# Optimization experiments

Hardware: AMD Instinct MI355X
Metric: run time of the kernel (lower is better)

The kernel has to match this reference:

```python
import jax, jax.numpy as jnp
import numpy as np

EPS = 1e-5
NUM_GROUPS = 16


def _deform_conv(x, offset, mask, weight):
    """Modulated deformable conv v2, 3x3, stride 1, pad 1, no bias.
    x: [B,C,H,W], offset: [B,18,H,W] (y,x interleaved per kernel point),
    mask: [B,9,H,W], weight: [O,C,3,3].
    """
    B, C, H, W = x.shape
    O = weight.shape[0]
    K = 9
    off = offset.reshape(B, K, 2, H, W)
    dy, dx = off[:, :, 0], off[:, :, 1]  # [B,K,H,W]
    # base sampling grid: output pixel + kernel tap offset (pad=1 -> taps -1..1)
    ky, kx = jnp.meshgrid(jnp.arange(3), jnp.arange(3), indexing='ij')
    ky = (ky.reshape(K) - 1).astype(x.dtype)
    kx = (kx.reshape(K) - 1).astype(x.dtype)
    iy = jnp.arange(H, dtype=x.dtype)[:, None]
    ix = jnp.arange(W, dtype=x.dtype)[None, :]
    py = iy[None, None] + ky[None, :, None, None] + dy  # [B,K,H,W]
    px = ix[None, None] + kx[None, :, None, None] + dx

    y0 = jnp.floor(py)
    x0 = jnp.floor(px)
    wy = py - y0  # grad flows to offsets via these weights
    wx = px - x0

    xf = x.reshape(B, C, H * W)

    def gather(yc, xc, w):
        # yc,xc,w: [B,K,H,W] float; returns weighted samples [B,C,K,H,W]
        valid = (yc >= 0) & (yc <= H - 1) & (xc >= 0) & (xc <= W - 1)
        yi = jnp.clip(yc, 0, H - 1).astype(jnp.int32)
        xi = jnp.clip(xc, 0, W - 1).astype(jnp.int32)
        idx = (yi * W + xi).reshape(B, K * H * W)
        g = jax.vmap(lambda xb, ib: xb[:, ib])(xf, idx)  # [B,C,K*H*W]
        g = g.reshape(B, C, K, H, W)
        wv = (w * valid.astype(x.dtype))[:, None]  # [B,1,K,H,W]
        return g * wv

    val = gather(y0, x0, (1 - wy) * (1 - wx))
    val = val + gather(y0, x0 + 1, (1 - wy) * wx)
    val = val + gather(y0 + 1, x0, wy * (1 - wx))
    val = val + gather(y0 + 1, x0 + 1, wy * wx)

    val = val * mask[:, None]  # modulation: [B,C,K,H,W] * [B,1,K,H,W]
    w = weight.reshape(O, C, K)
    return jnp.einsum('bckhw,ock->bohw', val, w)


def _group_norm(y, gamma, beta):
    B, O, H, W = y.shape
    g = y.reshape(B, NUM_GROUPS, O // NUM_GROUPS, H, W)
    mean = g.mean(axis=(2, 3, 4), keepdims=True)
    var = ((g - mean) ** 2).mean(axis=(2, 3, 4), keepdims=True)
    g = (g - mean) * jax.lax.rsqrt(var + EPS)
    y = g.reshape(B, O, H, W)
    return y * gamma[None, :, None, None] + beta[None, :, None, None]


def setup_inputs() -> dict:
    key = jax.random.key(0)
    k1, k2, k3, k4 = jax.random.split(key, 4)
    B, C, O, H, W = 8, 256, 256, 64, 64
    x = jax.random.normal(k1, (B, C, H, W), jnp.float32)
    offset = jax.random.normal(k2, (B, 18, H, W), jnp.float32)
    mask = jax.random.uniform(k3, (B, 9, H, W), jnp.float32)
    weight = jax.random.normal(k4, (O, C, 3, 3), jnp.float32) * 0.02
    gamma = jnp.ones((O,), jnp.float32)
    beta = jnp.zeros((O,), jnp.float32)
    return {"x": x, "offset": offset, "mask": mask, "weight": weight,
            "gamma": gamma, "beta": beta}


def reference(x, offset, mask, weight, gamma, beta):
    y = _deform_conv(x, offset, mask, weight)
    return _group_norm(y, gamma, beta)
```

## Files before the change

### kernel.cpp

```cpp
#include <hip/hip_runtime.h>
#include <hip/hip_fp16.h>
#include <math.h>

#define BB 8
#define CC 256
#define OO 256
#define HH 64
#define WW 64
#define KK 9
#define HWSZ 4096
#define CKSZ 2304
#define NG 16
#define OPG 16
#define EPSV 1e-5f

typedef _Float16 f16;
typedef f16 f16x8 __attribute__((ext_vector_type(8)));
typedef float f32x4 __attribute__((ext_vector_type(4)));

#define XH_ELEMS ((size_t)BB*HWSZ*CC)
#define WF_ELEMS ((size_t)OO*CKSZ)
#define CV_ELEMS ((size_t)BB*OO*HWSZ)
#define NSTRIP 32

__global__ __launch_bounds__(256) void x_transpose_k(
    const float* __restrict__ x, __half* __restrict__ xh)
{
  int blk = blockIdx.x;
  int b = blk >> 8; int rem = blk & 255;
  int c0 = (rem >> 6) * 64; int hw0 = (rem & 63) * 64;
  __shared__ float st[64][65];
  int t = threadIdx.x;
  #pragma unroll
  for (int i = 0; i < 16; ++i) {
    int idx = t + i*256; int c = idx >> 6, w = idx & 63;
    st[c][w] = x[((size_t)(b*CC + c0 + c))*HWSZ + hw0 + w];
  }
  __syncthreads();
  #pragma unroll
  for (int i = 0; i < 8; ++i) {
    int idx = t + i*256; int r = idx >> 5, cp = idx & 31;
    __half2 v = __floats2half2_rn(st[cp*2][r], st[cp*2+1][r]);
    *(__half2*)&xh[((size_t)(b*HWSZ) + hw0 + r)*CC + c0 + cp*2] = v;
  }
}

__global__ __launch_bounds__(256) void w_frag_k(
    const float* __restrict__ w, __half* __restrict__ wf)
{
  int i = blockIdx.x*256 + threadIdx.x;
  int e = i & 7, lane = (i >> 3) & 63, mi = (i >> 9) & 3;
  int ks = (i >> 11) & 1, wm = (i >> 12) & 3, cc = i >> 14;
  int k = cc >> 2, c0i = cc & 3;
  int o = wm*64 + mi*16 + (lane & 15);
  int c = c0i*64 + ks*32 + (lane >> 4)*8 + e;
  wf[i] = __float2half(w[(o*CC + c)*KK + k]);
}

template<int F16OUT>
__global__ __launch_bounds__(512, 2) void dcn_mfma_k(
    const float* __restrict__ off, const float* __restrict__ msk,
    const __half* __restrict__ xh, const __half* __restrict__ wf,
    float* __restrict__ out32, __half* __restrict__ conv16,
    float* __restrict__ psum)
{
  __shared__ __half sVl[2][128*64];
  __shared__ uint   sTapP[KK][128][4];

  const int t = threadIdx.x;
  const int b = blockIdx.x & 7;
  const int strip = blockIdx.x >> 3;
  const int h0 = strip * 2;

  const int lane = t & 63, wid = t >> 6;
  const int lr = lane & 15, lh = lane >> 4;
  const int gp = t >> 2, gq = t & 3;

  auto load_A = [&](int cc, f16x8 a[2][2]) {
    #pragma unroll
    for (int ks = 0; ks < 2; ++ks)
      #pragma unroll
      for (int mi = 0; mi < 2; ++mi) {
        int omi = wid*2 + mi;
        const __half* ap = wf + (size_t)(cc*4 + (omi >> 2))*4096
                              + (size_t)(ks*4 + (omi & 3))*512 + lane*8;
        a[ks][mi] = *(const f16x8*)ap;
      }
  };

  f16x8 aregA[2][2], aregB[2][2];
  load_A(0, aregA);

  for (int s = t; s < KK*128; s += 512) {
    int k = s >> 7, p = s & 127;
    int h = h0 + (p >> 6), w = p & 63;
    float dy = off[(((b*18) + 2*k    )*HH + h)*WW + w];
    float dx = off[(((b*18) + 2*k + 1)*HH + h)*WW + w];
    float m  = msk[(((b*KK) + k)*HH + h)*WW + w];
    float py = (float)(h + (k/3) - 1) + dy;
    float px = (float)(w + (k%3) - 1) + dx;
    float y0f = floorf(py), x0f = floorf(px);
    float wy = py - y0f, wx = px - x0f;
    int y0 = (int)y0f, x0 = (int)x0f;
    #pragma unroll
    for (int tap = 0; tap < 4; ++tap) {
      int yy = y0 + (tap >> 1), xx = x0 + (tap & 1);
      bool v = (yy >= 0) & (yy < HH) & (xx >= 0) & (xx < WW);
      float bw = ((tap >> 1) ? wy : 1.f - wy) * ((tap & 1) ? wx : 1.f - wx);
      float wgt = v ? bw * m : 0.f;
      int cy = min(max(yy, 0), HH-1), cx = min(max(xx, 0), WW-1);
      uint idx = (uint)(cy*WW + cx);
      sTapP[k][p][tap] = (idx << 16)
                       | (uint)__half_as_ushort(__float2half(wgt));
    }
  }
  __syncthreads();

  f32x4 acc[2][8];
  #pragma unroll
  for (int mi = 0; mi < 2; ++mi)
    #pragma unroll
    for (int ni = 0; ni < 8; ++ni) acc[mi][ni] = (f32x4){0.f,0.f,0.f,0.f};

  const char* xbase = (const char*)xh + (size_t)b * (HWSZ*CC*2);

  uint toff[4]; __half2 twv[4];
  #pragma unroll
  for (int i = 0; i < 4; ++i) {
    uint tp = sTapP[0][gp][i];
    toff[i] = (tp >> 16) << 9;
    twv[i]  = __half2half2(__ushort_as_half((unsigned short)(tp & 0xFFFFu)));
  }
  int tk = 0;

  auto combine_write = [&](uint4 r0, uint4 r1, uint4 r2, uint4 r3,
                           int oct, __half* dst) {
    const __half2* t0 = (const __half2*)&r0; const __half2* t1 = (const __half2*)&r1;
    const __half2* t2 = (const __half2*)&r2; const __half2* t3 = (const __half2*)&r3;
    __half2 o_[4];
    #pragma unroll
    for (int r = 0; r < 4; ++r)
      o_[r] = __hfma2(twv[0], t0[r], __hfma2(twv[1], t1[r],
              __hfma2(twv[2], t2[r], __hmul2(twv[3], t3[r]))));
    *(uint4*)&dst[gp*64 + ((oct ^ (gp & 7)) << 3)] = *(uint4*)o_;
  };

  {
    const char* cb = xbase + gq*16;
    uint4 a0 = *(const uint4*)(cb + toff[0]);
    uint4 a1 = *(const uint4*)(cb + toff[1]);
    uint4 a2 = *(const uint4*)(cb + toff[2]);
    uint4 a3 = *(const uint4*)(cb + toff[3]);
    uint4 b0 = *(const uint4*)(cb + toff[0] + 64);
    uint4 b1 = *(const uint4*)(cb + toff[1] + 64);
    uint4 b2 = *(const uint4*)(cb + toff[2] + 64);
    uint4 b3 = *(const uint4*)(cb + toff[3] + 64);
    combine_write(a0, a1, a2, a3, gq,     sVl[0]);
    combine_write(b0, b1, b2, b3, gq + 4, sVl[0]);
  }

  int cur = 0;

  auto do_chunk = [&](int cc, f16x8 aCur[2][2], f16x8 aNxt[2][2]) {
    __syncthreads();

    bool pf = (cc + 1 < 36);
    int kn = (cc+1) >> 2, c0n = ((cc+1) & 3) << 6;
    uint4 ga0, ga1, ga2, ga3, gb0, gb1, gb2, gb3;
    if (pf) {
      load_A(cc + 1, aNxt);
      if (kn != tk) {
        #pragma unroll
        for (int i = 0; i < 4; ++i) {
          uint tp = sTapP[kn][gp][i];
          toff[i] = (tp >> 16) << 9;
          twv[i]  = __half2half2(__ushort_as_half((unsigned short)(tp & 0xFFFFu)));
        }
        tk = kn;
      }
      const char* cb = xbase + (size_t)(c0n*2) + gq*16;
      ga0 = *(const uint4*)(cb + toff[0]);
      ga1 = *(const uint4*)(cb + toff[1]);
      ga2 = *(const uint4*)(cb + toff[2]);
      ga3 = *(const uint4*)(cb + toff[3]);
      gb0 = *(const uint4*)(cb + toff[0] + 64);
      gb1 = *(const uint4*)(cb + toff[1] + 64);
      gb2 = *(const uint4*)(cb + toff[2] + 64);
      gb3 = *(const uint4*)(cb + toff[3] + 64);
    }

    #pragma unroll
    for (int ks = 0; ks < 2; ++ks) {
      f16x8 brg[8];
      #pragma unroll
      for (int ni = 0; ni < 8; ++ni) {
        int r = ni*16 + lr;
        brg[ni] = *(const f16x8*)&sVl[cur][r*64 + (((ks*4 + lh) ^ (r & 7)) << 3)];
      }
      #pragma unroll
      for (int mi = 0; mi < 2; ++mi)
        #pragma unroll
        for (int ni = 0; ni < 8; ++ni)
          acc[mi][ni] = __builtin_amdgcn_mfma_f32_16x16x32_f16(
              aCur[ks][mi], brg[ni], acc[mi][ni], 0, 0, 0);
    }

    if (pf) {
      combine_write(ga0, ga1, ga2, ga3, gq,     sVl[cur ^ 1]);
      combine_write(gb0, gb1, gb2, gb3, gq + 4, sVl[cur ^ 1]);
      cur ^= 1;
    }
  };

  #pragma unroll 1
  for (int cc2 = 0; cc2 < 36; cc2 += 2) {
    do_chunk(cc2,     aregA, aregB);
    do_chunk(cc2 + 1, aregB, aregA);
  }

  #pragma unroll
  for (int mi = 0; mi < 2; ++mi) {
    #pragma unroll
    for (int ni = 0; ni < 8; ++ni) {
      int ob = wid*32 + mi*16 + lh*4;
      int pp = ni*16 + lr;
      #pragma unroll
      for (int j = 0; j < 4; ++j) {
        size_t idx = ((size_t)(b*OO + ob + j))*HWSZ + strip*128 + pp;
        if (F16OUT) conv16[idx] = __float2half(acc[mi][ni][j]);
        else        out32[idx] = acc[mi][ni][j];
      }
    }
  }

  if (F16OUT) {
    #pragma unroll
    for (int mi = 0; mi < 2; ++mi) {
      float s1 = 0.f, s2 = 0.f;
      #pragma unroll
      for (int ni = 0; ni < 8; ++ni)
        #pragma unroll
        for (int j = 0; j < 4; ++j) {
          float v = acc[mi][ni][j];
          s1 += v; s2 += v*v;
        }
      #pragma unroll
      for (int d = 32; d > 0; d >>= 1) {
        s1 += __shfl_xor(s1, d);
        s2 += __shfl_xor(s2, d);
      }
      if (lane == 0) {
        int g = wid*2 + mi;
        psum[(size_t)blockIdx.x*32 + g*2]     = s1;
        psum[(size_t)blockIdx.x*32 + g*2 + 1] = s2;
      }
    }
  }
}

__global__ __launch_bounds__(256) void gn_norm2_k(
    const __half* __restrict__ conv16, const float* __restrict__ psum,
    const float* __restrict__ gamma, const float* __restrict__ beta,
    float* __restrict__ out)
{
  int bid = blockIdx.x;
  int bo = bid >> 1;
  int b = bo >> 8, o = bo & 255;
  int g = o >> 4;
  float s1 = 0.f, s2 = 0.f;
  for (int st = 0; st < NSTRIP; ++st) {
    s1 += psum[(size_t)(st*8 + b)*32 + g*2];
    s2 += psum[(size_t)(st*8 + b)*32 + g*2 + 1];
  }
  const float invN = 1.f / (float)(OPG*HWSZ);
  float mean = s1 * invN;
  float var  = s2 * invN - mean*mean;
  float inv = rsqrtf(var + EPSV);
  float sc = gamma[o]*inv;
  float sh = beta[o] - mean*sc;

  size_t e0 = ((size_t)(b*OO + o))*HWSZ + (size_t)(bid & 1)*2048
            + (size_t)threadIdx.x*8;
  uint4 u = *(const uint4*)(conv16 + e0);
  const __half2* hh = (const __half2*)&u;
  float r[8];
  #pragma unroll
  for (int j = 0; j < 4; ++j) {
    float2 f = __half22float2(hh[j]);
    r[2*j] = f.x; r[2*j+1] = f.y;
  }
  *(float4*)&out[e0]     = make_float4(r[0]*sc+sh, r[1]*sc+sh, r[2]*sc+sh, r[3]*sc+sh);
  *(float4*)&out[e0 + 4] = make_float4(r[4]*sc+sh, r[5]*sc+sh, r[6]*sc+sh, r[7]*sc+sh);
}

__global__ __launch_bounds__(1024) void gn_stats_k(
    const float* __restrict__ out, float* __restrict__ stats)
{
  int bg = blockIdx.x;
  const float4* p = (const float4*)(out + (size_t)bg*OPG*HWSZ);
  const int n4 = OPG*HWSZ/4;
  float s1 = 0.f, s2 = 0.f;
  for (int i = threadIdx.x; i < n4; i += 1024) {
    float4 v = p[i];
    s1 += v.x + v.y + v.z + v.w;
    s2 += v.x*v.x + v.y*v.y + v.z*v.z + v.w*v.w;
  }
  #pragma unroll
  for (int o2 = 32; o2 > 0; o2 >>= 1) {
    s1 += __shfl_down(s1, o2);
    s2 += __shfl_down(s2, o2);
  }
  __shared__ float r1[16], r2[16];
  int wd = threadIdx.x >> 6, lane = threadIdx.x & 63;
  if (lane == 0) { r1[wd] = s1; r2[wd] = s2; }
  __syncthreads();
  if (threadIdx.x == 0) {
    float t1 = 0.f, t2 = 0.f;
    #pragma unroll
    for (int i = 0; i < 16; i++) { t1 += r1[i]; t2 += r2[i]; }
    const float invN = 1.f / (float)(OPG*HWSZ);
    float mean = t1 * invN;
    float var  = t2 * invN - mean*mean;
    stats[bg*2]   = mean;
    stats[bg*2+1] = var;
  }
}

__global__ __launch_bounds__(256) void gn_norm_k(
    float* __restrict__ out, const float* __restrict__ stats,
    const float* __restrict__ gamma, const float* __restrict__ beta)
{
  size_t i = (size_t)blockIdx.x*256 + threadIdx.x;
  const size_t n4 = (size_t)BB*OO*HWSZ/4;
  if (i >= n4) return;
  size_t base = i*4;
  int bo = (int)(base / HWSZ);
  int b = bo / OO, o = bo - b*OO;
  int g = o >> 4;
  float mean = stats[(b*NG+g)*2], var = stats[(b*NG+g)*2+1];
  float inv = rsqrtf(var + EPSV);
  float sc = gamma[o]*inv;
  float sh = beta[o] - mean*sc;
  float4 v = *(float4*)&out[base];
  v.x = v.x*sc + sh; v.y = v.y*sc + sh;
  v.z = v.z*sc + sh; v.w = v.w*sc + sh;
  *(float4*)&out[base] = v;
}

extern "C" void kernel_launch(void* const* d_in, const int* in_sizes, int n_in,
                              void* d_out, int out_size, void* d_ws, size_t ws_size,
                              hipStream_t stream) {
  const float* x      = (const float*)d_in[0];
  const float* offset = (const float*)d_in[1];
  const float* mask   = (const float*)d_in[2];
  const float* weight = (const float*)d_in[3];
  const float* gamma  = (const float*)d_in[4];
  const float* beta   = (const float*)d_in[5];
  float* out = (float*)d_out;

  __half* xh   = (__half*)d_ws;
  __half* wf   = xh + XH_ELEMS;
  __half* cv   = wf + WF_ELEMS;
  float* psum  = (float*)(cv + CV_ELEMS);

  const size_t need = (XH_ELEMS + WF_ELEMS + CV_ELEMS)*2
                    + (size_t)BB*NSTRIP*32*4 + 1024;

  x_transpose_k<<<BB*4*64, 256, 0, stream>>>(x, xh);
  w_frag_k<<<(int)(WF_ELEMS/256), 256, 0, stream>>>(weight, wf);

  if (ws_size >= need) {
    dcn_mfma_k<1><<<BB*NSTRIP, 512, 0, stream>>>(offset, mask, xh, wf,
                                                 (float*)nullptr, cv, psum);
    gn_norm2_k<<<4096, 256, 0, stream>>>(cv, psum, gamma, beta, out);
  } else {
    float* stats = (float*)(wf + WF_ELEMS);
    dcn_mfma_k<0><<<BB*NSTRIP, 512, 0, stream>>>(offset, mask, xh, wf,
                                                 out, (__half*)nullptr,
                                                 (float*)nullptr);
    gn_stats_k<<<BB*NG, 1024, 0, stream>>>(out, stats);
    gn_norm_k<<<(int)((size_t)BB*OO*HWSZ/4 + 255)/256, 256, 0, stream>>>(
        out, stats, gamma, beta);
  }
}
```

Before: 81.92 us.

## Deepen LDS gather pipeline to four buffers with one barrier per chunk pair

The shared-memory ring for gathered deformable samples grows from two to four buffers, so prefetching runs two chunks ahead and `__syncthreads` runs once per pair of chunks instead of once per chunk. Weight fragments are now loaded two chunks ahead, right after the compute that frees their registers. The aim is to cut barrier stalls and hide gather latency behind the MFMA work. The cost is doubled LDS per block, about 82KB in total. That likely no longer lets two 512-thread blocks fit per CU as `launch_bounds` requests, which would reduce occupancy.

```diff
diff --git a/kernel.cpp b/kernel.cpp
--- a/kernel.cpp
+++ b/kernel.cpp
@@ -64,7 +64,7 @@
     float* __restrict__ out32, __half* __restrict__ conv16,
     float* __restrict__ psum)
 {
-  __shared__ __half sVl[2][128*64];
+  __shared__ __half sVl[4][128*64];
   __shared__ uint   sTapP[KK][128][4];
 
   const int t = threadIdx.x;
@@ -90,6 +90,7 @@
 
   f16x8 aregA[2][2], aregB[2][2];
   load_A(0, aregA);
+  load_A(1, aregB);
 
   for (int s = t; s < KK*128; s += 512) {
     int k = s >> 7, p = s & 127;
@@ -145,8 +146,18 @@
     *(uint4*)&dst[gp*64 + ((oct ^ (gp & 7)) << 3)] = *(uint4*)o_;
   };
 
-  {
-    const char* cb = xbase + gq*16;
+  auto gather_chunk = [&](int cc, __half* dst) {
+    int kn = cc >> 2, c0n = (cc & 3) << 6;
+    if (kn != tk) {
+      #pragma unroll
+      for (int i = 0; i < 4; ++i) {
+        uint tp = sTapP[kn][gp][i];
+        toff[i] = (tp >> 16) << 9;
+        twv[i]  = __half2half2(__ushort_as_half((unsigned short)(tp & 0xFFFFu)));
+      }
+      tk = kn;
+    }
+    const char* cb = xbase + (size_t)(c0n*2) + gq*16;
     uint4 a0 = *(const uint4*)(cb + toff[0]);
     uint4 a1 = *(const uint4*)(cb + toff[1]);
     uint4 a2 = *(const uint4*)(cb + toff[2]);
@@ -155,20 +166,18 @@
     uint4 b1 = *(const uint4*)(cb + toff[1] + 64);
     uint4 b2 = *(const uint4*)(cb + toff[2] + 64);
     uint4 b3 = *(const uint4*)(cb + toff[3] + 64);
-    combine_write(a0, a1, a2, a3, gq,     sVl[0]);
-    combine_write(b0, b1, b2, b3, gq + 4, sVl[0]);
-  }
-
-  int cur = 0;
-
-  auto do_chunk = [&](int cc, f16x8 aCur[2][2], f16x8 aNxt[2][2]) {
-    __syncthreads();
-
-    bool pf = (cc + 1 < 36);
-    int kn = (cc+1) >> 2, c0n = ((cc+1) & 3) << 6;
+    combine_write(a0, a1, a2, a3, gq,     dst);
+    combine_write(b0, b1, b2, b3, gq + 4, dst);
+  };
+
+  gather_chunk(0, sVl[0]);
+  gather_chunk(1, sVl[1]);
+
+  auto do_half = [&](int ccm, int ccf, f16x8 aCur[2][2]) {
+    bool pf = (ccf < 36);
+    int kn = ccf >> 2, c0n = (ccf & 3) << 6;
     uint4 ga0, ga1, ga2, ga3, gb0, gb1, gb2, gb3;
     if (pf) {
-      load_A(cc + 1, aNxt);
       if (kn != tk) {
         #pragma unroll
         for (int i = 0; i < 4; ++i) {
@@ -189,13 +198,14 @@
       gb3 = *(const uint4*)(cb + toff[3] + 64);
     }
 
+    const __half* vb = sVl[ccm & 3];
     #pragma unroll
     for (int ks = 0; ks < 2; ++ks) {
       f16x8 brg[8];
       #pragma unroll
       for (int ni = 0; ni < 8; ++ni) {
         int r = ni*16 + lr;
-        brg[ni] = *(const f16x8*)&sVl[cur][r*64 + (((ks*4 + lh) ^ (r & 7)) << 3)];
+        brg[ni] = *(const f16x8*)&vb[r*64 + (((ks*4 + lh) ^ (r & 7)) << 3)];
       }
       #pragma unroll
       for (int mi = 0; mi < 2; ++mi)
@@ -206,16 +216,18 @@
     }
 
     if (pf) {
-      combine_write(ga0, ga1, ga2, ga3, gq,     sVl[cur ^ 1]);
-      combine_write(gb0, gb1, gb2, gb3, gq + 4, sVl[cur ^ 1]);
-      cur ^= 1;
+      __half* dst = sVl[ccf & 3];
+      combine_write(ga0, ga1, ga2, ga3, gq,     dst);
+      combine_write(gb0, gb1, gb2, gb3, gq + 4, dst);
+      load_A(ccf, aCur);
     }
   };
 
   #pragma unroll 1
-  for (int cc2 = 0; cc2 < 36; cc2 += 2) {
-    do_chunk(cc2,     aregA, aregB);
-    do_chunk(cc2 + 1, aregB, aregA);
+  for (int ccp = 0; ccp < 36; ccp += 2) {
+    __syncthreads();
+    do_half(ccp,     ccp + 2, aregA);
+    do_half(ccp + 1, ccp + 3, aregB);
   }
 
   #pragma unroll
```

New measurement: 80.88 us. Within noise of the previous version (-1.3%).
